# Optimization experiments

Hardware: AMD Instinct MI355X
Metric: run time of the kernel (lower is better)

The kernel has to match this reference:

```python
import jax, jax.numpy as jnp
import numpy as np

WS = 7   # window size
NH = 6   # num heads

def layer_norm(x, g, b, eps=1e-5):
    m = x.mean(-1, keepdims=True)
    v = ((x - m) ** 2).mean(-1, keepdims=True)
    return (x - m) / jnp.sqrt(v + eps) * g + b

def rel_pos_index(ws):
    coords = np.stack(np.meshgrid(np.arange(ws), np.arange(ws), indexing='ij')).reshape(2, -1)
    rel = (coords[:, :, None] - coords[:, None, :]).transpose(1, 2, 0)
    rel[:, :, 0] += ws - 1
    rel[:, :, 1] += ws - 1
    rel[:, :, 0] *= 2 * ws - 1
    return rel.sum(-1)  # (ws*ws, ws*ws) numpy int

RPI = rel_pos_index(WS)

def window_partition(x, ws):
    B, H, W, C = x.shape
    return x.reshape(B, H // ws, ws, W // ws, ws, C).transpose(0, 1, 3, 2, 4, 5).reshape(-1, ws * ws, C)

def window_reverse(w, ws, B, H, W):
    return w.reshape(B, H // ws, W // ws, ws, ws, -1).transpose(0, 1, 3, 2, 4, 5).reshape(B, H, W, -1)

def make_attn_mask(H, W, ws, shift):
    # Swin shifted-window mask (constant, computed in numpy)
    img = np.zeros((1, H, W, 1), np.float32)
    cnt = 0
    for h in (slice(0, -ws), slice(-ws, -shift), slice(-shift, None)):
        for w in (slice(0, -ws), slice(-ws, -shift), slice(-shift, None)):
            img[:, h, w, :] = cnt
            cnt += 1
    mw = img.reshape(1, H // ws, ws, W // ws, ws, 1).transpose(0, 1, 3, 2, 4, 5).reshape(-1, ws * ws)
    m = mw[:, None, :] - mw[:, :, None]
    return jnp.asarray(np.where(m != 0, -100.0, 0.0).astype(np.float32))  # (nW, N, N)

def conv2d(x, w, b, padding):
    y = jax.lax.conv_general_dilated(x, w, (1, 1), padding, dimension_numbers=('NCHW', 'OIHW', 'NCHW'))
    return y + b[None, :, None, None]

def swin_block(x, H, W, shift, n1g, n1b, qkvw, qkvb, projw, projb, rel, n2g, n2b, f1w, f1b, f2w, f2b):
    B, L, C = x.shape
    hd = C // NH
    shortcut = x
    x = layer_norm(x, n1g, n1b).reshape(B, H, W, C)
    if shift > 0:
        x = jnp.roll(x, (-shift, -shift), axis=(1, 2))
    xw = window_partition(x, WS)            # (B*nW, N, C)
    nWB, N, _ = xw.shape
    qkv = (xw @ qkvw.T + qkvb).reshape(nWB, N, 3, NH, hd).transpose(2, 0, 3, 1, 4)
    q, k, v = qkv[0] * (hd ** -0.5), qkv[1], qkv[2]
    attn = jnp.einsum('whnd,whmd->whnm', q, k)
    attn = attn + rel[RPI].transpose(2, 0, 1)[None]   # relative position bias (NH,N,N)
    if shift > 0:
        mask = make_attn_mask(H, W, WS, shift)        # (nW, N, N)
        nW = mask.shape[0]
        attn = (attn.reshape(B, nW, NH, N, N) + mask[None, :, None]).reshape(nWB, NH, N, N)
    attn = jax.nn.softmax(attn, axis=-1)
    xw = jnp.einsum('whnm,whmd->wnhd', attn, v).reshape(nWB, N, C)
    xw = xw @ projw.T + projb
    x = window_reverse(xw, WS, B, H, W)
    if shift > 0:
        x = jnp.roll(x, (shift, shift), axis=(1, 2))
    x = shortcut + x.reshape(B, L, C)
    h = layer_norm(x, n2g, n2b)
    h = jax.nn.gelu(h @ f1w.T + f1b, approximate=False) @ f2w.T + f2b
    return x + h

def setup_inputs() -> dict:
    key = jax.random.key(0)
    ks = iter(jax.random.split(key, 32))
    B, C, H, W = 8, 192, 56, 56
    C2, hid = C // 2, 4 * (C // 2)
    rn = lambda shape, s=0.02: jax.random.normal(next(ks), shape, jnp.float32) * s
    return dict(
        x=jax.random.normal(next(ks), (B, C, H, W), jnp.float32),
        up_w=rn((C2, C, 3, 3)), up_b=jnp.zeros((C2,), jnp.float32),
        bn_g=jnp.ones((C2,), jnp.float32), bn_b=jnp.zeros((C2,), jnp.float32),
        bn_mean=jnp.zeros((C2,), jnp.float32), bn_var=jnp.ones((C2,), jnp.float32),
        n1g=jnp.ones((2, C2), jnp.float32), n1b=jnp.zeros((2, C2), jnp.float32),
        qkv_w=rn((2, 3 * C2, C2)), qkv_b=jnp.zeros((2, 3 * C2), jnp.float32),
        proj_w=rn((2, C2, C2)), proj_b=jnp.zeros((2, C2), jnp.float32),
        rel=rn((2, (2 * WS - 1) ** 2, NH)),
        n2g=jnp.ones((2, C2), jnp.float32), n2b=jnp.zeros((2, C2), jnp.float32),
        f1w=rn((2, hid, C2)), f1b=jnp.zeros((2, hid), jnp.float32),
        f2w=rn((2, C2, hid)), f2b=jnp.zeros((2, C2), jnp.float32),
        out_w=rn((C // 4, C2, 1, 1)), out_b=jnp.zeros((C // 4,), jnp.float32),
    )

def reference(x, up_w, up_b, bn_g, bn_b, bn_mean, bn_var, n1g, n1b, qkv_w, qkv_b, proj_w, proj_b, rel, n2g, n2b, f1w, f1b, f2w, f2b, out_w, out_b):
    B, C, H, W = x.shape
    x = jnp.repeat(jnp.repeat(x, 2, axis=2), 2, axis=3)
    x = conv2d(x, up_w, up_b, 'SAME')
    x = (x - bn_mean[None, :, None, None]) * (bn_g / jnp.sqrt(bn_var + 1e-5))[None, :, None, None] + bn_b[None, :, None, None]
    x = jax.nn.relu(x)
    H2, W2, C2 = 2 * H, 2 * W, C // 2
    t = x.reshape(B, C2, H2 * W2).transpose(0, 2, 1)   # (B, L, C2)
    for i, shift in enumerate((0, WS // 2)):
        t = swin_block(t, H2, W2, shift, n1g[i], n1b[i], qkv_w[i], qkv_b[i], proj_w[i], proj_b[i], rel[i], n2g[i], n2b[i], f1w[i], f1b[i], f2w[i], f2b[i])
    x = t.transpose(0, 2, 1).reshape(B, C2, H2, W2)
    return jax.nn.relu(conv2d(x, out_w, out_b, 'VALID'))
```

## Files before the change

kernel.cpp:

```cpp
#include <hip/hip_runtime.h>
#include <math.h>

#define M_TOK 100352
#define NHEAD 6

typedef unsigned short u16;
typedef __attribute__((ext_vector_type(8))) short bf16x8;
typedef __attribute__((ext_vector_type(4))) float f32x4;
typedef __attribute__((ext_vector_type(4))) unsigned int u32x4;

__device__ inline u16 f2bf(float f) {
    union { float f; unsigned int i; } v; v.f = f;
    unsigned int r = v.i + 0x7fffu + ((v.i >> 16) & 1u);
    return (u16)(r >> 16);
}

__global__ __launch_bounds__(256) void cast_w_kernel(const float* __restrict__ qkvw,
        const float* __restrict__ projw, const float* __restrict__ f1w,
        const float* __restrict__ f2w, const float* __restrict__ outw,
        u16* __restrict__ Wh) {
    int i = blockIdx.x * 256 + threadIdx.x;
    if (i < 55296) Wh[i] = f2bf(qkvw[i]);
    else if (i < 73728) Wh[i] = f2bf(projw[i - 55296]);
    else if (i < 147456) Wh[i] = f2bf(f1w[i - 73728]);
    else if (i < 221184) Wh[i] = f2bf(f2w[i - 147456]);
    else if (i < 225792) Wh[i] = f2bf(outw[i - 221184]);
}

__global__ __launch_bounds__(256) void fold_kernel(const float* __restrict__ up_w,
                                                   u16* __restrict__ Wc) {
    int idx = blockIdx.x * 256 + threadIdx.x;
    if (idx >= 96 * 4 * 192) return;
    int c2 = idx / 768;
    int rem = idx - c2 * 768;
    int p = rem / 192;
    int ci = rem - p * 192;
    int po = p >> 1, pw = p & 1;
    const float* w = up_w + (c2 * 192 + ci) * 9;
    float w9[9];
#pragma unroll
    for (int k = 0; k < 9; k++) w9[k] = w[k];
    float r0[3], r1[3];
#pragma unroll
    for (int kw = 0; kw < 3; kw++) {
        if (po == 0) { r0[kw] = w9[kw];              r1[kw] = w9[3 + kw] + w9[6 + kw]; }
        else         { r0[kw] = w9[kw] + w9[3 + kw]; r1[kw] = w9[6 + kw]; }
    }
    float o00, o01, o10, o11;
    if (pw == 0) { o00 = r0[0];         o01 = r0[1] + r0[2]; o10 = r1[0];         o11 = r1[1] + r1[2]; }
    else         { o00 = r0[0] + r0[1]; o01 = r0[2];         o10 = r1[0] + r1[1]; o11 = r1[2]; }
    size_t base = ((size_t)p * 4 * 96 + c2) * 192 + ci;
    Wc[base + 0 * 96 * 192] = f2bf(o00);
    Wc[base + 1 * 96 * 192] = f2bf(o01);
    Wc[base + 2 * 96 * 192] = f2bf(o10);
    Wc[base + 3 * 96 * 192] = f2bf(o11);
}

__global__ __launch_bounds__(256) void bias_gen(const float* __restrict__ rel,
                                                float* __restrict__ BT) {
    int blkid = blockIdx.x;
    int blk = blkid / 24;
    int rem = blkid - blk * 24;
    int type = rem / 6, head = rem - (rem / 6) * 6;
    const float* relp = rel + blk * 1014;
    bool shift = (blk == 1);
    for (int i = threadIdx.x; i < 4096; i += 256) {
        int a = i >> 6, k = i & 63;
        float v;
        if (k >= 49) v = -1e30f;
        else if (a >= 49) v = 0.f;
        else {
            int ah = (a * 37) >> 8, aw = a - ah * 7;
            int kh = (k * 37) >> 8, kw = k - kh * 7;
            v = relp[((ah - kh + 6) * 13 + (aw - kw + 6)) * 6 + head];
            if (shift) {
                int lha = (type & 2) ? (ah < 4 ? 1 : 2) : 0;
                int lwa = (type & 1) ? (aw < 4 ? 1 : 2) : 0;
                int lhk = (type & 2) ? (kh < 4 ? 1 : 2) : 0;
                int lwk = (type & 1) ? (kw < 4 ? 1 : 2) : 0;
                if (lha != lhk || lwa != lwk) v -= 100.f;
            }
        }
        BT[(size_t)blkid * 4096 + i] = v;
    }
}

__global__ __launch_bounds__(256) void transpose_kernel(const float* __restrict__ x,
                                                        u16* __restrict__ xT) {
    __shared__ unsigned int ts[64 * 96];
    int b = blockIdx.y;
    int pix0 = blockIdx.x * 64;
    int tid = threadIdx.x;
    int p = tid & 63, dg = tid >> 6;
    const float* xb = x + (size_t)b * 192 * 3136 + pix0 + p;
    for (int d = dg; d < 96; d += 4) {
        float v0 = xb[(size_t)(2 * d) * 3136];
        float v1 = xb[(size_t)(2 * d + 1) * 3136];
        unsigned int pk = ((unsigned int)f2bf(v1) << 16) | (unsigned int)f2bf(v0);
        ts[p * 96 + ((d & ~31) | ((d & 31) ^ (p & 31)))] = pk;
    }
    __syncthreads();
    for (int i = tid; i < 1536; i += 256) {
        int pp = i / 24, c = i - pp * 24;
        unsigned int r[4];
#pragma unroll
        for (int j = 0; j < 4; j++) {
            int d = c * 4 + j;
            r[j] = ts[pp * 96 + ((d & ~31) | ((d & 31) ^ (pp & 31)))];
        }
        u32x4 v = {r[0], r[1], r[2], r[3]};
        *(u32x4*)&xT[((size_t)b * 3136 + pix0 + pp) * 192 + c * 8] = v;
    }
}

__global__ __launch_bounds__(256) void conv_mfma(const u16* __restrict__ xT,
        const u16* __restrict__ Wc, const float* __restrict__ up_b,
        const float* __restrict__ bn_g, const float* __restrict__ bn_b,
        const float* __restrict__ bn_m, const float* __restrict__ bn_v,
        const float* __restrict__ lg, const float* __restrict__ lb,
        float* __restrict__ T, u16* __restrict__ XBh) {
    __shared__ u16 xs[81 * 200];
    __shared__ __align__(16) u16 ws[96 * 104];
    int tile = blockIdx.x, p = blockIdx.y, b = blockIdx.z;
    int po = p >> 1, pw = p & 1;
    int a0 = (tile / 7) * 8, b0 = (tile % 7) * 8;
    int rro = a0 - 1 + po, cco = b0 - 1 + pw;
    int tid = threadIdx.x;
    int w = tid >> 6, lane = tid & 63, quad = lane >> 4, l16 = lane & 15;
    int mbase = (w & 1) * 32;
    int nt0 = (w >> 1) * 3;
    int half = w >> 1;

    for (int i = tid; i < 1944; i += 256) {
        int pix = i / 24, c = i - pix * 24;
        int rr = pix / 9, cc = pix - rr * 9;
        int gr = rro + rr, gc = cco + cc;
        u32x4 v = {0u, 0u, 0u, 0u};
        if ((unsigned)gr < 56u && (unsigned)gc < 56u)
            v = *(const u32x4*)&xT[((size_t)b * 3136 + gr * 56 + gc) * 192 + c * 8];
        *(u32x4*)&xs[pix * 200 + c * 8] = v;
    }

    f32x4 acc[2][3];
#pragma unroll
    for (int mi = 0; mi < 2; mi++)
#pragma unroll
        for (int ni = 0; ni < 3; ni++) acc[mi][ni] = f32x4{0.f, 0.f, 0.f, 0.f};

    int aoffp[2];
#pragma unroll
    for (int mi = 0; mi < 2; mi++) {
        int pixel = mbase + mi * 16 + l16;
        aoffp[mi] = ((pixel >> 3) * 9 + (pixel & 7)) * 200;
    }

    for (int tap = 0; tap < 4; tap++) {
        int di = tap >> 1, dj = tap & 1;
        int tsh = (di * 9 + dj) * 200;
        for (int kc = 0; kc < 2; kc++) {
            __syncthreads();
            for (int i = tid; i < 1152; i += 256) {
                int r = i / 12, c = i - r * 12;
                *(u32x4*)&ws[r * 104 + c * 8] =
                    *(const u32x4*)&Wc[(((size_t)p * 4 + tap) * 96 + r) * 192 + kc * 96 + c * 8];
            }
            __syncthreads();
#pragma unroll
            for (int kk = 0; kk < 3; kk++) {
                bf16x8 af[2], bfr[3];
#pragma unroll
                for (int mi = 0; mi < 2; mi++)
                    af[mi] = *(const bf16x8*)&xs[aoffp[mi] + tsh + kc * 96 + kk * 32 + quad * 8];
#pragma unroll
                for (int ni = 0; ni < 3; ni++)
                    bfr[ni] = *(const bf16x8*)&ws[((nt0 + ni) * 16 + l16) * 104 + kk * 32 + quad * 8];
#pragma unroll
                for (int mi = 0; mi < 2; mi++)
#pragma unroll
                    for (int ni = 0; ni < 3; ni++)
                        acc[mi][ni] = __builtin_amdgcn_mfma_f32_16x16x32_bf16(
                            af[mi], bfr[ni], acc[mi][ni], 0, 0, 0);
            }
        }
    }

#pragma unroll
    for (int ni = 0; ni < 3; ni++) {
        int c2 = (nt0 + ni) * 16 + l16;
        float sc = bn_g[c2] * rsqrtf(bn_v[c2] + 1e-5f);
        float sh = (up_b[c2] - bn_m[c2]) * sc + bn_b[c2];
#pragma unroll
        for (int mi = 0; mi < 2; mi++) {
#pragma unroll
            for (int reg = 0; reg < 4; reg++) {
                int pixel = mbase + mi * 16 + quad * 4 + reg;
                int pr = pixel >> 3, pc = pixel & 7;
                int oh = 2 * (a0 + pr) + po, ow = 2 * (b0 + pc) + pw;
                size_t tok = (size_t)b * 12544 + oh * 112 + ow;
                float v = fmaxf(acc[mi][ni][reg] * sc + sh, 0.f);
                acc[mi][ni][reg] = v;
                T[tok * 96 + c2] = v;
            }
        }
    }

    float sA[2][4], qA[2][4];
#pragma unroll
    for (int mi = 0; mi < 2; mi++)
#pragma unroll
        for (int reg = 0; reg < 4; reg++) {
            float s = acc[mi][0][reg] + acc[mi][1][reg] + acc[mi][2][reg];
            float q = acc[mi][0][reg] * acc[mi][0][reg] + acc[mi][1][reg] * acc[mi][1][reg]
                    + acc[mi][2][reg] * acc[mi][2][reg];
#pragma unroll
            for (int d = 1; d < 16; d <<= 1) {
                s += __shfl_xor(s, d, 64);
                q += __shfl_xor(q, d, 64);
            }
            sA[mi][reg] = s; qA[mi][reg] = q;
        }
    __syncthreads();
    float2* parts = (float2*)ws;
    if (l16 == 0) {
#pragma unroll
        for (int mi = 0; mi < 2; mi++)
#pragma unroll
            for (int reg = 0; reg < 4; reg++) {
                int pixel = mbase + mi * 16 + quad * 4 + reg;
                parts[pixel * 2 + half] = make_float2(sA[mi][reg], qA[mi][reg]);
            }
    }
    __syncthreads();
    float gcl[3], bcl[3];
#pragma unroll
    for (int ni = 0; ni < 3; ni++) {
        int c2 = (nt0 + ni) * 16 + l16;
        gcl[ni] = lg[c2]; bcl[ni] = lb[c2];
    }
#pragma unroll
    for (int mi = 0; mi < 2; mi++)
#pragma unroll
        for (int reg = 0; reg < 4; reg++) {
            int pixel = mbase + mi * 16 + quad * 4 + reg;
            float2 oth = parts[pixel * 2 + (half ^ 1)];
            float ts_ = sA[mi][reg] + oth.x, tq = qA[mi][reg] + oth.y;
            float mean = ts_ * (1.f / 96.f);
            float var = tq * (1.f / 96.f) - mean * mean;
            float rstd = rsqrtf(var + 1e-5f);
            int pr = pixel >> 3, pc = pixel & 7;
            int oh = 2 * (a0 + pr) + po, ow = 2 * (b0 + pc) + pw;
            size_t tok = (size_t)b * 12544 + oh * 112 + ow;
#pragma unroll
            for (int ni = 0; ni < 3; ni++) {
                int c2 = (nt0 + ni) * 16 + l16;
                XBh[tok * 96 + c2] = f2bf((acc[mi][ni][reg] - mean) * rstd * gcl[ni] + bcl[ni]);
            }
        }
}

template <int EPI>
__global__ __launch_bounds__(256) void gemm_act(const u16* __restrict__ Xh,
        const u16* __restrict__ W, const float* __restrict__ bias,
        u16* __restrict__ Cout, int N) {
    __shared__ u16 Xs[128 * 104];
    __shared__ u16 Ws[96 * 104];
    int tid = threadIdx.x;
    int w = tid >> 6, lane = tid & 63, quad = lane >> 4, l16 = lane & 15;
    int mh = w & 1, nh = w >> 1;
    int n0 = blockIdx.x * 96;
    size_t m0 = (size_t)blockIdx.y * 128;

    for (int i = tid; i < 1536; i += 256) {
        int r = i / 12, c = i - r * 12;
        *(u32x4*)&Xs[r * 104 + c * 8] = *(const u32x4*)&Xh[(m0 + r) * 96 + c * 8];
    }
    for (int i = tid; i < 1152; i += 256) {
        int r = i / 12, c = i - r * 12;
        *(u32x4*)&Ws[r * 104 + c * 8] = *(const u32x4*)&W[(size_t)(n0 + r) * 96 + c * 8];
    }
    __syncthreads();

    f32x4 acc[3][4];
#pragma unroll
    for (int ni = 0; ni < 3; ni++)
#pragma unroll
        for (int mi = 0; mi < 4; mi++) acc[ni][mi] = f32x4{0.f, 0.f, 0.f, 0.f};
#pragma unroll
    for (int kk = 0; kk < 3; kk++) {
        bf16x8 af[3], bf[4];
#pragma unroll
        for (int ni = 0; ni < 3; ni++)
            af[ni] = *(const bf16x8*)&Ws[(nh * 48 + ni * 16 + l16) * 104 + kk * 32 + quad * 8];
#pragma unroll
        for (int mi = 0; mi < 4; mi++)
            bf[mi] = *(const bf16x8*)&Xs[(mh * 64 + mi * 16 + l16) * 104 + kk * 32 + quad * 8];
#pragma unroll
        for (int ni = 0; ni < 3; ni++)
#pragma unroll
            for (int mi = 0; mi < 4; mi++)
                acc[ni][mi] = __builtin_amdgcn_mfma_f32_16x16x32_bf16(
                    af[ni], bf[mi], acc[ni][mi], 0, 0, 0);
    }

#pragma unroll
    for (int ni = 0; ni < 3; ni++) {
        int colb = n0 + nh * 48 + ni * 16 + quad * 4;
        float4 bv = *(const float4*)&bias[colb];
#pragma unroll
        for (int mi = 0; mi < 4; mi++) {
            size_t row = m0 + mh * 64 + mi * 16 + l16;
            float v0 = acc[ni][mi][0] + bv.x, v1 = acc[ni][mi][1] + bv.y;
            float v2 = acc[ni][mi][2] + bv.z, v3 = acc[ni][mi][3] + bv.w;
            if (EPI == 1) {
                v0 = 0.5f * v0 * (1.f + erff(v0 * 0.70710678118654752f));
                v1 = 0.5f * v1 * (1.f + erff(v1 * 0.70710678118654752f));
                v2 = 0.5f * v2 * (1.f + erff(v2 * 0.70710678118654752f));
                v3 = 0.5f * v3 * (1.f + erff(v3 * 0.70710678118654752f));
            }
            unsigned int d0 = ((unsigned int)f2bf(v1) << 16) | f2bf(v0);
            unsigned int d1 = ((unsigned int)f2bf(v3) << 16) | f2bf(v2);
            *(uint2*)&Cout[row * N + colb] = make_uint2(d0, d1);
        }
    }
}

template <int LNM>
__global__ __launch_bounds__(256) void gemm_res(const u16* __restrict__ Xh,
        const u16* __restrict__ W, const float* __restrict__ bias,
        const float* __restrict__ res, float* __restrict__ Tout,
        const float* __restrict__ g, const float* __restrict__ bt,
        u16* __restrict__ Yh, int K) {
    __shared__ __align__(16) u16 Xs[128 * 104];
    __shared__ u16 Ws[96 * 104];
    int tid = threadIdx.x;
    int w = tid >> 6, lane = tid & 63, quad = lane >> 4, l16 = lane & 15;
    int mh = w & 1, nh = w >> 1;
    size_t m0 = (size_t)blockIdx.x * 128;

    f32x4 acc[3][4];
#pragma unroll
    for (int ni = 0; ni < 3; ni++)
#pragma unroll
        for (int mi = 0; mi < 4; mi++) acc[ni][mi] = f32x4{0.f, 0.f, 0.f, 0.f};

    for (int k0 = 0; k0 < K; k0 += 96) {
        __syncthreads();
        for (int i = tid; i < 1536; i += 256) {
            int r = i / 12, c = i - r * 12;
            *(u32x4*)&Xs[r * 104 + c * 8] = *(const u32x4*)&Xh[(m0 + r) * K + k0 + c * 8];
        }
        for (int i = tid; i < 1152; i += 256) {
            int r = i / 12, c = i - r * 12;
            *(u32x4*)&Ws[r * 104 + c * 8] = *(const u32x4*)&W[(size_t)r * K + k0 + c * 8];
        }
        __syncthreads();
#pragma unroll
        for (int kk = 0; kk < 3; kk++) {
            bf16x8 af[3], bf[4];
#pragma unroll
            for (int ni = 0; ni < 3; ni++)
                af[ni] = *(const bf16x8*)&Ws[(nh * 48 + ni * 16 + l16) * 104 + kk * 32 + quad * 8];
#pragma unroll
            for (int mi = 0; mi < 4; mi++)
                bf[mi] = *(const bf16x8*)&Xs[(mh * 64 + mi * 16 + l16) * 104 + kk * 32 + quad * 8];
#pragma unroll
            for (int ni = 0; ni < 3; ni++)
#pragma unroll
                for (int mi = 0; mi < 4; mi++)
                    acc[ni][mi] = __builtin_amdgcn_mfma_f32_16x16x32_bf16(
                        af[ni], bf[mi], acc[ni][mi], 0, 0, 0);
        }
    }

#pragma unroll
    for (int ni = 0; ni < 3; ni++) {
        int colb = nh * 48 + ni * 16 + quad * 4;
        float4 bv = *(const float4*)&bias[colb];
#pragma unroll
        for (int mi = 0; mi < 4; mi++) {
            size_t row = m0 + mh * 64 + mi * 16 + l16;
            float4 rv = *(const float4*)&res[row * 96 + colb];
            acc[ni][mi][0] += bv.x + rv.x;
            acc[ni][mi][1] += bv.y + rv.y;
            acc[ni][mi][2] += bv.z + rv.z;
            acc[ni][mi][3] += bv.w + rv.w;
            *(f32x4*)&Tout[row * 96 + colb] = acc[ni][mi];
        }
    }

    if (LNM == 1) {
        float sm4[4], qm4[4];
#pragma unroll
        for (int mi = 0; mi < 4; mi++) {
            float s = 0.f, q = 0.f;
#pragma unroll
            for (int ni = 0; ni < 3; ni++)
#pragma unroll
                for (int r = 0; r < 4; r++) {
                    float v = acc[ni][mi][r];
                    s += v; q += v * v;
                }
            s += __shfl_xor(s, 16, 64); s += __shfl_xor(s, 32, 64);
            q += __shfl_xor(q, 16, 64); q += __shfl_xor(q, 32, 64);
            sm4[mi] = s; qm4[mi] = q;
        }
        __syncthreads();
        float2* parts = (float2*)Xs;
        if (quad == 0) {
#pragma unroll
            for (int mi = 0; mi < 4; mi++)
                parts[(mh * 64 + mi * 16 + l16) * 2 + nh] = make_float2(sm4[mi], qm4[mi]);
        }
        __syncthreads();
        float mean4[4], rstd4[4];
#pragma unroll
        for (int mi = 0; mi < 4; mi++) {
            float2 oth = parts[(mh * 64 + mi * 16 + l16) * 2 + (nh ^ 1)];
            float ts_ = sm4[mi] + oth.x, tq = qm4[mi] + oth.y;
            float mean = ts_ * (1.f / 96.f);
            float var = tq * (1.f / 96.f) - mean * mean;
            mean4[mi] = mean;
            rstd4[mi] = rsqrtf(var + 1e-5f);
        }
#pragma unroll
        for (int ni = 0; ni < 3; ni++) {
            int colb = nh * 48 + ni * 16 + quad * 4;
            float4 g4 = *(const float4*)&g[colb];
            float4 b4 = *(const float4*)&bt[colb];
#pragma unroll
            for (int mi = 0; mi < 4; mi++) {
                size_t row = m0 + mh * 64 + mi * 16 + l16;
                float y0 = (acc[ni][mi][0] - mean4[mi]) * rstd4[mi] * g4.x + b4.x;
                float y1 = (acc[ni][mi][1] - mean4[mi]) * rstd4[mi] * g4.y + b4.y;
                float y2 = (acc[ni][mi][2] - mean4[mi]) * rstd4[mi] * g4.z + b4.z;
                float y3 = (acc[ni][mi][3] - mean4[mi]) * rstd4[mi] * g4.w + b4.w;
                unsigned int d0 = ((unsigned int)f2bf(y1) << 16) | f2bf(y0);
                unsigned int d1 = ((unsigned int)f2bf(y3) << 16) | f2bf(y2);
                *(uint2*)&Yh[row * 96 + colb] = make_uint2(d0, d1);
            }
        }
    } else {
#pragma unroll
        for (int ni = 0; ni < 3; ni++) {
            int colb = nh * 48 + ni * 16 + quad * 4;
#pragma unroll
            for (int mi = 0; mi < 4; mi++) {
                size_t row = m0 + mh * 64 + mi * 16 + l16;
                unsigned int d0 = ((unsigned int)f2bf(acc[ni][mi][1]) << 16) | f2bf(acc[ni][mi][0]);
                unsigned int d1 = ((unsigned int)f2bf(acc[ni][mi][3]) << 16) | f2bf(acc[ni][mi][2]);
                *(uint2*)&Yh[row * 96 + colb] = make_uint2(d0, d1);
            }
        }
    }
}

__global__ __launch_bounds__(192, 3) void attn_mfma(const u16* __restrict__ qkv,
        const float* __restrict__ BT, u16* __restrict__ ao, int shift) {
    __shared__ u16 Pl[3][64 * 72];
    __shared__ u16 vts[3][16 * 72];

    int tid = threadIdx.x;
    int w = tid >> 6, lane = tid & 63, quad = lane >> 4, l16 = lane & 15;
    int Wd = blockIdx.x;
    int bb = Wd >> 8, wl = Wd & 255, wh = wl >> 4, ww = wl & 15;
    int type = ((wh == 15) ? 2 : 0) + ((ww == 15) ? 1 : 0);

    int toks4[4], tokV;
#pragma unroll
    for (int t = 0; t < 4; t++) {
        int a = t * 16 + l16; if (a > 48) a = 48;
        int r = (a * 37) >> 8, c = a - r * 7;
        int h = wh * 7 + r, wq = ww * 7 + c;
        if (shift) { h += 3; if (h >= 112) h -= 112; wq += 3; if (wq >= 112) wq -= 112; }
        toks4[t] = bb * 12544 + h * 112 + wq;
    }
    {
        int a = lane > 48 ? 48 : lane;
        int r = (a * 37) >> 8, c = a - r * 7;
        int h = wh * 7 + r, wq = ww * 7 + c;
        if (shift) { h += 3; if (h >= 112) h -= 112; wq += 3; if (wq >= 112) wq -= 112; }
        tokV = bb * 12544 + h * 112 + wq;
    }

    u16* Pw = Pl[w];
    u16* vw = vts[w];

    for (int i = lane; i < 240; i += 64) {
        int rrow = i / 15, key = 49 + (i - rrow * 15);
        vw[rrow * 72 + key] = 0;
    }

    for (int hh = 0; hh < 2; hh++) {
        int head = w * 2 + hh;

        union { u32x4 u; bf16x8 h; } qf[4], kf[4];
#pragma unroll
        for (int t = 0; t < 4; t++) {
            u32x4 zq = {0u, 0u, 0u, 0u}, zk = {0u, 0u, 0u, 0u};
            if (quad < 2) {
                const u16* rb = qkv + (size_t)toks4[t] * 288 + head * 16 + quad * 8;
                zq = *(const u32x4*)(rb);
                zk = *(const u32x4*)(rb + 96);
            }
            qf[t].u = zq; kf[t].u = zk;
        }

        if (lane < 49) {
            const u16* vb = qkv + (size_t)tokV * 288 + head * 16 + 192;
            union { u32x4 v; unsigned int u[4]; } v0, v1;
            v0.v = *(const u32x4*)(vb);
            v1.v = *(const u32x4*)(vb + 8);
#pragma unroll
            for (int j = 0; j < 4; j++) {
                vw[(2 * j) * 72 + lane]         = (u16)(v0.u[j] & 0xffffu);
                vw[(2 * j + 1) * 72 + lane]     = (u16)(v0.u[j] >> 16);
                vw[(8 + 2 * j) * 72 + lane]     = (u16)(v1.u[j] & 0xffffu);
                vw[(8 + 2 * j + 1) * 72 + lane] = (u16)(v1.u[j] >> 16);
            }
        }

        f32x4 S[4][4];
#pragma unroll
        for (int kt = 0; kt < 4; kt++)
#pragma unroll
            for (int qt = 0; qt < 4; qt++)
                S[kt][qt] = __builtin_amdgcn_mfma_f32_16x16x32_bf16(
                    kf[kt].h, qf[qt].h, f32x4{0.f, 0.f, 0.f, 0.f}, 0, 0, 0);

        const float* bbase = BT + (size_t)(type * 6 + head) * 4096;
        float rinv[4];
#pragma unroll
        for (int qt = 0; qt < 4; qt++) {
            f32x4 bv[4];
#pragma unroll
            for (int kt = 0; kt < 4; kt++)
                bv[kt] = *(const f32x4*)&bbase[(size_t)(qt * 16 + l16) * 64 + kt * 16 + quad * 4];
            float mx = -3e38f;
#pragma unroll
            for (int kt = 0; kt < 4; kt++)
#pragma unroll
                for (int r = 0; r < 4; r++) {
                    float v = fmaf(S[kt][qt][r], 0.25f, bv[kt][r]);
                    S[kt][qt][r] = v;
                    mx = fmaxf(mx, v);
                }
            mx = fmaxf(mx, __shfl_xor(mx, 16, 64));
            mx = fmaxf(mx, __shfl_xor(mx, 32, 64));
            float sm = 0.f;
#pragma unroll
            for (int kt = 0; kt < 4; kt++)
#pragma unroll
                for (int r = 0; r < 4; r++) {
                    float e = __expf(S[kt][qt][r] - mx);
                    S[kt][qt][r] = e;
                    sm += e;
                }
            sm += __shfl_xor(sm, 16, 64);
            sm += __shfl_xor(sm, 32, 64);
            rinv[qt] = 1.0f / sm;
        }

#pragma unroll
        for (int qt = 0; qt < 4; qt++)
#pragma unroll
            for (int kt = 0; kt < 4; kt++) {
                unsigned int d0 = ((unsigned int)f2bf(S[kt][qt][1]) << 16) | f2bf(S[kt][qt][0]);
                unsigned int d1 = ((unsigned int)f2bf(S[kt][qt][3]) << 16) | f2bf(S[kt][qt][2]);
                *(uint2*)&Pw[(qt * 16 + l16) * 72 + kt * 16 + quad * 4] = make_uint2(d0, d1);
            }

        bf16x8 vf[2];
#pragma unroll
        for (int ksp = 0; ksp < 2; ksp++)
            vf[ksp] = *(const bf16x8*)&vw[l16 * 72 + ksp * 32 + quad * 8];
#pragma unroll
        for (int qt = 0; qt < 4; qt++) {
            f32x4 O = {0.f, 0.f, 0.f, 0.f};
#pragma unroll
            for (int ksp = 0; ksp < 2; ksp++) {
                bf16x8 pf = *(const bf16x8*)&Pw[(qt * 16 + l16) * 72 + ksp * 32 + quad * 8];
                O = __builtin_amdgcn_mfma_f32_16x16x32_bf16(vf[ksp], pf, O, 0, 0, 0);
            }
            int a = qt * 16 + l16;
            if (a < 49) {
                float ri = rinv[qt];
                unsigned int d0 = ((unsigned int)f2bf(O[1] * ri) << 16) | f2bf(O[0] * ri);
                unsigned int d1 = ((unsigned int)f2bf(O[3] * ri) << 16) | f2bf(O[2] * ri);
                *(uint2*)&ao[(size_t)toks4[qt] * 96 + head * 16 + quad * 4] = make_uint2(d0, d1);
            }
        }
    }
}

__global__ __launch_bounds__(256) void outconv_mfma(const u16* __restrict__ Th,
        const u16* __restrict__ Woc, const float* __restrict__ ob,
        float* __restrict__ out) {
    __shared__ u16 Xs[128 * 104];
    __shared__ u16 Ws[48 * 104];
    int tid = threadIdx.x;
    int w = tid >> 6, lane = tid & 63, quad = lane >> 4, l16 = lane & 15;
    int t0 = blockIdx.x * 128, b = blockIdx.y;
    size_t m0 = (size_t)b * 12544 + t0;

    for (int i = tid; i < 576; i += 256) {
        int r = i / 12, c = i - r * 12;
        *(u32x4*)&Ws[r * 104 + c * 8] = *(const u32x4*)&Woc[(size_t)r * 96 + c * 8];
    }
    for (int i = tid; i < 1536; i += 256) {
        int r = i / 12, c = i - r * 12;
        *(u32x4*)&Xs[r * 104 + c * 8] = *(const u32x4*)&Th[(m0 + r) * 96 + c * 8];
    }
    __syncthreads();

    f32x4 acc[2][3];
#pragma unroll
    for (int mi = 0; mi < 2; mi++)
#pragma unroll
        for (int ni = 0; ni < 3; ni++) acc[mi][ni] = f32x4{0.f, 0.f, 0.f, 0.f};
#pragma unroll
    for (int kk = 0; kk < 3; kk++) {
        bf16x8 af[2], bfr[3];
#pragma unroll
        for (int mi = 0; mi < 2; mi++)
            af[mi] = *(const bf16x8*)&Xs[(w * 32 + mi * 16 + l16) * 104 + kk * 32 + quad * 8];
#pragma unroll
        for (int ni = 0; ni < 3; ni++)
            bfr[ni] = *(const bf16x8*)&Ws[(ni * 16 + l16) * 104 + kk * 32 + quad * 8];
#pragma unroll
        for (int mi = 0; mi < 2; mi++)
#pragma unroll
            for (int ni = 0; ni < 3; ni++)
                acc[mi][ni] = __builtin_amdgcn_mfma_f32_16x16x32_bf16(
                    af[mi], bfr[ni], acc[mi][ni], 0, 0, 0);
    }

#pragma unroll
    for (int mi = 0; mi < 2; mi++)
#pragma unroll
        for (int ni = 0; ni < 3; ni++) {
            int co = ni * 16 + l16;
            float bb = ob[co];
            f32x4 o = {fmaxf(acc[mi][ni][0] + bb, 0.f), fmaxf(acc[mi][ni][1] + bb, 0.f),
                       fmaxf(acc[mi][ni][2] + bb, 0.f), fmaxf(acc[mi][ni][3] + bb, 0.f)};
            *(f32x4*)&out[((size_t)b * 48 + co) * 12544 + t0 + w * 32 + mi * 16 + quad * 4] = o;
        }
}

extern "C" void kernel_launch(void* const* d_in, const int* in_sizes, int n_in,
                              void* d_out, int out_size, void* d_ws, size_t ws_size,
                              hipStream_t stream) {
    const float* x     = (const float*)d_in[0];
    const float* up_w  = (const float*)d_in[1];
    const float* up_b  = (const float*)d_in[2];
    const float* bn_g  = (const float*)d_in[3];
    const float* bn_b  = (const float*)d_in[4];
    const float* bn_m  = (const float*)d_in[5];
    const float* bn_v  = (const float*)d_in[6];
    const float* n1g   = (const float*)d_in[7];
    const float* n1b   = (const float*)d_in[8];
    const float* qkvw  = (const float*)d_in[9];
    const float* qkvb  = (const float*)d_in[10];
    const float* projw = (const float*)d_in[11];
    const float* projb = (const float*)d_in[12];
    const float* rel   = (const float*)d_in[13];
    const float* n2g   = (const float*)d_in[14];
    const float* n2b   = (const float*)d_in[15];
    const float* f1w   = (const float*)d_in[16];
    const float* f1b   = (const float*)d_in[17];
    const float* f2w   = (const float*)d_in[18];
    const float* f2b   = (const float*)d_in[19];
    const float* outw  = (const float*)d_in[20];
    const float* outb  = (const float*)d_in[21];
    float* out = (float*)d_out;

    char* base = (char*)d_ws;
    float* T  = (float*)base;                       base += (size_t)M_TOK * 96 * 4;
    u16* XBh  = (u16*)base;                         base += (size_t)M_TOK * 96 * 2;
    u16* BIGh = (u16*)base;                         base += (size_t)M_TOK * 384 * 2;
    u16* xT   = (u16*)base;                         base += (size_t)8 * 3136 * 192 * 2;
    u16* Wc   = (u16*)base;                         base += (size_t)16 * 96 * 192 * 2;
    u16* Wh   = (u16*)base;                         base += (size_t)225792 * 2;
    float* BT = (float*)base;
    u16* qkvwh = Wh;
    u16* projwh = Wh + 55296;
    u16* f1wh = Wh + 73728;
    u16* f2wh = Wh + 147456;
    u16* outwh = Wh + 221184;

    cast_w_kernel<<<882, 256, 0, stream>>>(qkvw, projw, f1w, f2w, outw, Wh);
    fold_kernel<<<288, 256, 0, stream>>>(up_w, Wc);
    bias_gen<<<48, 256, 0, stream>>>(rel, BT);
    transpose_kernel<<<dim3(49, 8), 256, 0, stream>>>(x, xT);
    conv_mfma<<<dim3(49, 4, 8), 256, 0, stream>>>(xT, Wc, up_b, bn_g, bn_b, bn_m, bn_v,
                                                  n1g, n1b, T, XBh);

    for (int blk = 0; blk < 2; blk++) {
        int shift = (blk == 0) ? 0 : 3;
        gemm_act<0><<<dim3(3, M_TOK / 128), 256, 0, stream>>>(
            XBh, qkvwh + blk * 27648, qkvb + blk * 288, BIGh, 288);
        attn_mfma<<<2048, 192, 0, stream>>>(BIGh, BT + (size_t)blk * 98304, XBh, shift);
        gemm_res<1><<<M_TOK / 128, 256, 0, stream>>>(
            XBh, projwh + blk * 9216, projb + blk * 96, T, T,
            n2g + blk * 96, n2b + blk * 96, XBh, 96);
        gemm_act<1><<<dim3(4, M_TOK / 128), 256, 0, stream>>>(
            XBh, f1wh + blk * 36864, f1b + blk * 384, BIGh, 384);
        if (blk == 0) {
            gemm_res<1><<<M_TOK / 128, 256, 0, stream>>>(
                BIGh, f2wh + blk * 36864, f2b + blk * 96, T, T,
                n1g + 96, n1b + 96, XBh, 384);
        } else {
            gemm_res<0><<<M_TOK / 128, 256, 0, stream>>>(
                BIGh, f2wh + blk * 36864, f2b + blk * 96, T, T,
                nullptr, nullptr, XBh, 384);
        }
    }

    outconv_mfma<<<dim3(98, 8), 256, 0, stream>>>(XBh, outwh, outb, out);
}
```

Before: 611.5 us.

## Load GEMM operands directly from global into registers; merge prep kernels

```diff
diff --git a/kernel.cpp b/kernel.cpp
--- a/kernel.cpp
+++ b/kernel.cpp
@@ -15,73 +15,75 @@
     return (u16)(r >> 16);
 }
 
-__global__ __launch_bounds__(256) void cast_w_kernel(const float* __restrict__ qkvw,
+__global__ __launch_bounds__(256) void prep_kernel(const float* __restrict__ qkvw,
         const float* __restrict__ projw, const float* __restrict__ f1w,
         const float* __restrict__ f2w, const float* __restrict__ outw,
-        u16* __restrict__ Wh) {
-    int i = blockIdx.x * 256 + threadIdx.x;
-    if (i < 55296) Wh[i] = f2bf(qkvw[i]);
-    else if (i < 73728) Wh[i] = f2bf(projw[i - 55296]);
-    else if (i < 147456) Wh[i] = f2bf(f1w[i - 73728]);
-    else if (i < 221184) Wh[i] = f2bf(f2w[i - 147456]);
-    else if (i < 225792) Wh[i] = f2bf(outw[i - 221184]);
-}
-
-__global__ __launch_bounds__(256) void fold_kernel(const float* __restrict__ up_w,
-                                                   u16* __restrict__ Wc) {
-    int idx = blockIdx.x * 256 + threadIdx.x;
-    if (idx >= 96 * 4 * 192) return;
-    int c2 = idx / 768;
-    int rem = idx - c2 * 768;
-    int p = rem / 192;
-    int ci = rem - p * 192;
-    int po = p >> 1, pw = p & 1;
-    const float* w = up_w + (c2 * 192 + ci) * 9;
-    float w9[9];
-#pragma unroll
-    for (int k = 0; k < 9; k++) w9[k] = w[k];
-    float r0[3], r1[3];
-#pragma unroll
-    for (int kw = 0; kw < 3; kw++) {
-        if (po == 0) { r0[kw] = w9[kw];              r1[kw] = w9[3 + kw] + w9[6 + kw]; }
-        else         { r0[kw] = w9[kw] + w9[3 + kw]; r1[kw] = w9[6 + kw]; }
-    }
-    float o00, o01, o10, o11;
-    if (pw == 0) { o00 = r0[0];         o01 = r0[1] + r0[2]; o10 = r1[0];         o11 = r1[1] + r1[2]; }
-    else         { o00 = r0[0] + r0[1]; o01 = r0[2];         o10 = r1[0] + r1[1]; o11 = r1[2]; }
-    size_t base = ((size_t)p * 4 * 96 + c2) * 192 + ci;
-    Wc[base + 0 * 96 * 192] = f2bf(o00);
-    Wc[base + 1 * 96 * 192] = f2bf(o01);
-    Wc[base + 2 * 96 * 192] = f2bf(o10);
-    Wc[base + 3 * 96 * 192] = f2bf(o11);
-}
-
-__global__ __launch_bounds__(256) void bias_gen(const float* __restrict__ rel,
-                                                float* __restrict__ BT) {
-    int blkid = blockIdx.x;
-    int blk = blkid / 24;
-    int rem = blkid - blk * 24;
-    int type = rem / 6, head = rem - (rem / 6) * 6;
-    const float* relp = rel + blk * 1014;
-    bool shift = (blk == 1);
-    for (int i = threadIdx.x; i < 4096; i += 256) {
-        int a = i >> 6, k = i & 63;
-        float v;
-        if (k >= 49) v = -1e30f;
-        else if (a >= 49) v = 0.f;
-        else {
-            int ah = (a * 37) >> 8, aw = a - ah * 7;
-            int kh = (k * 37) >> 8, kw = k - kh * 7;
-            v = relp[((ah - kh + 6) * 13 + (aw - kw + 6)) * 6 + head];
-            if (shift) {
-                int lha = (type & 2) ? (ah < 4 ? 1 : 2) : 0;
-                int lwa = (type & 1) ? (aw < 4 ? 1 : 2) : 0;
-                int lhk = (type & 2) ? (kh < 4 ? 1 : 2) : 0;
-                int lwk = (type & 1) ? (kw < 4 ? 1 : 2) : 0;
-                if (lha != lhk || lwa != lwk) v -= 100.f;
-            }
-        }
-        BT[(size_t)blkid * 4096 + i] = v;
+        const float* __restrict__ up_w, const float* __restrict__ rel,
+        u16* __restrict__ Wh, u16* __restrict__ Wc, float* __restrict__ BT) {
+    int bid = blockIdx.x;
+    if (bid < 882) {
+        int i = bid * 256 + threadIdx.x;
+        if (i < 55296) Wh[i] = f2bf(qkvw[i]);
+        else if (i < 73728) Wh[i] = f2bf(projw[i - 55296]);
+        else if (i < 147456) Wh[i] = f2bf(f1w[i - 73728]);
+        else if (i < 221184) Wh[i] = f2bf(f2w[i - 147456]);
+        else if (i < 225792) Wh[i] = f2bf(outw[i - 221184]);
+        return;
+    }
+    if (bid < 1170) {
+        int idx = (bid - 882) * 256 + threadIdx.x;
+        if (idx >= 96 * 4 * 192) return;
+        int c2 = idx / 768;
+        int rem = idx - c2 * 768;
+        int p = rem / 192;
+        int ci = rem - p * 192;
+        int po = p >> 1, pw = p & 1;
+        const float* w = up_w + (c2 * 192 + ci) * 9;
+        float w9[9];
+#pragma unroll
+        for (int k = 0; k < 9; k++) w9[k] = w[k];
+        float r0[3], r1[3];
+#pragma unroll
+        for (int kw = 0; kw < 3; kw++) {
+            if (po == 0) { r0[kw] = w9[kw];              r1[kw] = w9[3 + kw] + w9[6 + kw]; }
+            else         { r0[kw] = w9[kw] + w9[3 + kw]; r1[kw] = w9[6 + kw]; }
+        }
+        float o00, o01, o10, o11;
+        if (pw == 0) { o00 = r0[0];         o01 = r0[1] + r0[2]; o10 = r1[0];         o11 = r1[1] + r1[2]; }
+        else         { o00 = r0[0] + r0[1]; o01 = r0[2];         o10 = r1[0] + r1[1]; o11 = r1[2]; }
+        size_t base = ((size_t)p * 4 * 96 + c2) * 192 + ci;
+        Wc[base + 0 * 96 * 192] = f2bf(o00);
+        Wc[base + 1 * 96 * 192] = f2bf(o01);
+        Wc[base + 2 * 96 * 192] = f2bf(o10);
+        Wc[base + 3 * 96 * 192] = f2bf(o11);
+        return;
+    }
+    {
+        int blkid = bid - 1170;
+        int blk = blkid / 24;
+        int rem = blkid - blk * 24;
+        int type = rem / 6, head = rem - (rem / 6) * 6;
+        const float* relp = rel + blk * 1014;
+        bool shift = (blk == 1);
+        for (int i = threadIdx.x; i < 4096; i += 256) {
+            int a = i >> 6, k = i & 63;
+            float v;
+            if (k >= 49) v = -1e30f;
+            else if (a >= 49) v = 0.f;
+            else {
+                int ah = (a * 37) >> 8, aw = a - ah * 7;
+                int kh = (k * 37) >> 8, kw = k - kh * 7;
+                v = relp[((ah - kh + 6) * 13 + (aw - kw + 6)) * 6 + head];
+                if (shift) {
+                    int lha = (type & 2) ? (ah < 4 ? 1 : 2) : 0;
+                    int lwa = (type & 1) ? (aw < 4 ? 1 : 2) : 0;
+                    int lhk = (type & 2) ? (kh < 4 ? 1 : 2) : 0;
+                    int lwk = (type & 1) ? (kw < 4 ? 1 : 2) : 0;
+                    if (lha != lhk || lwa != lwk) v -= 100.f;
+                }
+            }
+            BT[(size_t)blkid * 4096 + i] = v;
+        }
     }
 }
 
@@ -262,23 +264,23 @@
 __global__ __launch_bounds__(256) void gemm_act(const u16* __restrict__ Xh,
         const u16* __restrict__ W, const float* __restrict__ bias,
         u16* __restrict__ Cout, int N) {
-    __shared__ u16 Xs[128 * 104];
-    __shared__ u16 Ws[96 * 104];
     int tid = threadIdx.x;
     int w = tid >> 6, lane = tid & 63, quad = lane >> 4, l16 = lane & 15;
     int mh = w & 1, nh = w >> 1;
     int n0 = blockIdx.x * 96;
     size_t m0 = (size_t)blockIdx.y * 128;
 
-    for (int i = tid; i < 1536; i += 256) {
-        int r = i / 12, c = i - r * 12;
-        *(u32x4*)&Xs[r * 104 + c * 8] = *(const u32x4*)&Xh[(m0 + r) * 96 + c * 8];
-    }
-    for (int i = tid; i < 1152; i += 256) {
-        int r = i / 12, c = i - r * 12;
-        *(u32x4*)&Ws[r * 104 + c * 8] = *(const u32x4*)&W[(size_t)(n0 + r) * 96 + c * 8];
-    }
-    __syncthreads();
+    bf16x8 af[3][3], bf[4][3];
+#pragma unroll
+    for (int ni = 0; ni < 3; ni++)
+#pragma unroll
+        for (int kk = 0; kk < 3; kk++)
+            af[ni][kk] = *(const bf16x8*)&W[(size_t)(n0 + nh * 48 + ni * 16 + l16) * 96 + kk * 32 + quad * 8];
+#pragma unroll
+    for (int mi = 0; mi < 4; mi++)
+#pragma unroll
+        for (int kk = 0; kk < 3; kk++)
+            bf[mi][kk] = *(const bf16x8*)&Xh[(m0 + mh * 64 + mi * 16 + l16) * 96 + kk * 32 + quad * 8];
 
     f32x4 acc[3][4];
 #pragma unroll
@@ -286,21 +288,13 @@
 #pragma unroll
         for (int mi = 0; mi < 4; mi++) acc[ni][mi] = f32x4{0.f, 0.f, 0.f, 0.f};
 #pragma unroll
-    for (int kk = 0; kk < 3; kk++) {
-        bf16x8 af[3], bf[4];
-#pragma unroll
-        for (int ni = 0; ni < 3; ni++)
-            af[ni] = *(const bf16x8*)&Ws[(nh * 48 + ni * 16 + l16) * 104 + kk * 32 + quad * 8];
-#pragma unroll
-        for (int mi = 0; mi < 4; mi++)
-            bf[mi] = *(const bf16x8*)&Xs[(mh * 64 + mi * 16 + l16) * 104 + kk * 32 + quad * 8];
+    for (int kk = 0; kk < 3; kk++)
 #pragma unroll
         for (int ni = 0; ni < 3; ni++)
 #pragma unroll
             for (int mi = 0; mi < 4; mi++)
                 acc[ni][mi] = __builtin_amdgcn_mfma_f32_16x16x32_bf16(
-                    af[ni], bf[mi], acc[ni][mi], 0, 0, 0);
-    }
+                    af[ni][kk], bf[mi][kk], acc[ni][mi], 0, 0, 0);
 
 #pragma unroll
     for (int ni = 0; ni < 3; ni++) {
@@ -330,8 +324,7 @@
         const float* __restrict__ res, float* __restrict__ Tout,
         const float* __restrict__ g, const float* __restrict__ bt,
         u16* __restrict__ Yh, int K) {
-    __shared__ __align__(16) u16 Xs[128 * 104];
-    __shared__ u16 Ws[96 * 104];
+    __shared__ float2 parts[256];
     int tid = threadIdx.x;
     int w = tid >> 6, lane = tid & 63, quad = lane >> 4, l16 = lane & 15;
     int mh = w & 1, nh = w >> 1;
@@ -344,32 +337,25 @@
         for (int mi = 0; mi < 4; mi++) acc[ni][mi] = f32x4{0.f, 0.f, 0.f, 0.f};
 
     for (int k0 = 0; k0 < K; k0 += 96) {
-        __syncthreads();
-        for (int i = tid; i < 1536; i += 256) {
-            int r = i / 12, c = i - r * 12;
-            *(u32x4*)&Xs[r * 104 + c * 8] = *(const u32x4*)&Xh[(m0 + r) * K + k0 + c * 8];
-        }
-        for (int i = tid; i < 1152; i += 256) {
-            int r = i / 12, c = i - r * 12;
-            *(u32x4*)&Ws[r * 104 + c * 8] = *(const u32x4*)&W[(size_t)r * K + k0 + c * 8];
-        }
-        __syncthreads();
-#pragma unroll
-        for (int kk = 0; kk < 3; kk++) {
-            bf16x8 af[3], bf[4];
-#pragma unroll
-            for (int ni = 0; ni < 3; ni++)
-                af[ni] = *(const bf16x8*)&Ws[(nh * 48 + ni * 16 + l16) * 104 + kk * 32 + quad * 8];
-#pragma unroll
-            for (int mi = 0; mi < 4; mi++)
-                bf[mi] = *(const bf16x8*)&Xs[(mh * 64 + mi * 16 + l16) * 104 + kk * 32 + quad * 8];
+        bf16x8 af[3][3], bf[4][3];
+#pragma unroll
+        for (int ni = 0; ni < 3; ni++)
+#pragma unroll
+            for (int kk = 0; kk < 3; kk++)
+                af[ni][kk] = *(const bf16x8*)&W[(size_t)(nh * 48 + ni * 16 + l16) * K + k0 + kk * 32 + quad * 8];
+#pragma unroll
+        for (int mi = 0; mi < 4; mi++)
+#pragma unroll
+            for (int kk = 0; kk < 3; kk++)
+                bf[mi][kk] = *(const bf16x8*)&Xh[(m0 + mh * 64 + mi * 16 + l16) * K + k0 + kk * 32 + quad * 8];
+#pragma unroll
+        for (int kk = 0; kk < 3; kk++)
 #pragma unroll
             for (int ni = 0; ni < 3; ni++)
 #pragma unroll
                 for (int mi = 0; mi < 4; mi++)
                     acc[ni][mi] = __builtin_amdgcn_mfma_f32_16x16x32_bf16(
-                        af[ni], bf[mi], acc[ni][mi], 0, 0, 0);
-        }
+                        af[ni][kk], bf[mi][kk], acc[ni][mi], 0, 0, 0);
     }
 
 #pragma unroll
@@ -405,7 +391,6 @@
             sm4[mi] = s; qm4[mi] = q;
         }
         __syncthreads();
-        float2* parts = (float2*)Xs;
         if (quad == 0) {
 #pragma unroll
             for (int mi = 0; mi < 4; mi++)
@@ -595,22 +580,22 @@
 __global__ __launch_bounds__(256) void outconv_mfma(const u16* __restrict__ Th,
         const u16* __restrict__ Woc, const float* __restrict__ ob,
         float* __restrict__ out) {
-    __shared__ u16 Xs[128 * 104];
-    __shared__ u16 Ws[48 * 104];
     int tid = threadIdx.x;
     int w = tid >> 6, lane = tid & 63, quad = lane >> 4, l16 = lane & 15;
     int t0 = blockIdx.x * 128, b = blockIdx.y;
     size_t m0 = (size_t)b * 12544 + t0;
 
-    for (int i = tid; i < 576; i += 256) {
-        int r = i / 12, c = i - r * 12;
-        *(u32x4*)&Ws[r * 104 + c * 8] = *(const u32x4*)&Woc[(size_t)r * 96 + c * 8];
-    }
-    for (int i = tid; i < 1536; i += 256) {
-        int r = i / 12, c = i - r * 12;
-        *(u32x4*)&Xs[r * 104 + c * 8] = *(const u32x4*)&Th[(m0 + r) * 96 + c * 8];
-    }
-    __syncthreads();
+    bf16x8 af[2][3], bfr[3][3];
+#pragma unroll
+    for (int mi = 0; mi < 2; mi++)
+#pragma unroll
+        for (int kk = 0; kk < 3; kk++)
+            af[mi][kk] = *(const bf16x8*)&Th[(m0 + w * 32 + mi * 16 + l16) * 96 + kk * 32 + quad * 8];
+#pragma unroll
+    for (int ni = 0; ni < 3; ni++)
+#pragma unroll
+        for (int kk = 0; kk < 3; kk++)
+            bfr[ni][kk] = *(const bf16x8*)&Woc[(size_t)(ni * 16 + l16) * 96 + kk * 32 + quad * 8];
 
     f32x4 acc[2][3];
 #pragma unroll
@@ -618,21 +603,13 @@
 #pragma unroll
         for (int ni = 0; ni < 3; ni++) acc[mi][ni] = f32x4{0.f, 0.f, 0.f, 0.f};
 #pragma unroll
-    for (int kk = 0; kk < 3; kk++) {
-        bf16x8 af[2], bfr[3];
-#pragma unroll
-        for (int mi = 0; mi < 2; mi++)
-            af[mi] = *(const bf16x8*)&Xs[(w * 32 + mi * 16 + l16) * 104 + kk * 32 + quad * 8];
-#pragma unroll
-        for (int ni = 0; ni < 3; ni++)
-            bfr[ni] = *(const bf16x8*)&Ws[(ni * 16 + l16) * 104 + kk * 32 + quad * 8];
+    for (int kk = 0; kk < 3; kk++)
 #pragma unroll
         for (int mi = 0; mi < 2; mi++)
 #pragma unroll
             for (int ni = 0; ni < 3; ni++)
                 acc[mi][ni] = __builtin_amdgcn_mfma_f32_16x16x32_bf16(
-                    af[mi], bfr[ni], acc[mi][ni], 0, 0, 0);
-    }
+                    af[mi][kk], bfr[ni][kk], acc[mi][ni], 0, 0, 0);
 
 #pragma unroll
     for (int mi = 0; mi < 2; mi++)
@@ -687,9 +664,7 @@
     u16* f2wh = Wh + 147456;
     u16* outwh = Wh + 221184;
 
-    cast_w_kernel<<<882, 256, 0, stream>>>(qkvw, projw, f1w, f2w, outw, Wh);
-    fold_kernel<<<288, 256, 0, stream>>>(up_w, Wc);
-    bias_gen<<<48, 256, 0, stream>>>(rel, BT);
+    prep_kernel<<<1218, 256, 0, stream>>>(qkvw, projw, f1w, f2w, outw, up_w, rel, Wh, Wc, BT);
     transpose_kernel<<<dim3(49, 8), 256, 0, stream>>>(x, xT);
     conv_mfma<<<dim3(49, 4, 8), 256, 0, stream>>>(xT, Wc, up_b, bn_g, bn_b, bn_m, bn_v,
                                                   n1g, n1b, T, XBh);
```

New measurement: 597.7 us. -2.3%, faster.
